# Performance work log

Measured on AMD Instinct MI355X. Metric: run time of the kernel, lower is better.

The kernel has to match this reference:

```python
import jax, jax.numpy as jnp
import numpy as np

D_MODEL = 512
HEAD_NUM = 8
EPS = 1e-5


def setup_inputs() -> dict:
    key = jax.random.key(0)
    ks = jax.random.split(key, 7)
    B, S, D = 2, 4096, D_MODEL
    scale = 1.0 / np.sqrt(D)
    return {
        "x": jax.random.normal(ks[0], (B, S, D), dtype=jnp.float32),
        "Wq": jax.random.normal(ks[1], (D, D), dtype=jnp.float32) * scale,
        "bq": jnp.zeros((D,), dtype=jnp.float32),
        "Wk": jax.random.normal(ks[2], (D, D), dtype=jnp.float32) * scale,
        "bk": jnp.zeros((D,), dtype=jnp.float32),
        "Wv": jax.random.normal(ks[3], (D, D), dtype=jnp.float32) * scale,
        "bv": jnp.zeros((D,), dtype=jnp.float32),
        "gamma": jnp.ones((D,), dtype=jnp.float32),
        "beta": jnp.zeros((D,), dtype=jnp.float32),
    }


def reference(x, Wq, bq, Wk, bk, Wv, bv, gamma, beta):
    B, S, D = x.shape
    H = HEAD_NUM
    hd = D // H  # q_k_head_dim == v_head_dim == 64
    q = (x @ Wq + bq).reshape(B, H, S, hd)  # faithful to torch .view (no transpose)
    k = (x @ Wk + bk).reshape(B, H, S, hd)
    v = (x @ Wv + bv).reshape(B, H, S, hd)
    # [B,H,S,S] score matrix, materialized exactly as the original does
    scores = jnp.einsum("bhqd,bhkd->bhqk", q, k) / jnp.sqrt(jnp.float32(hd))
    attn_w = jax.nn.softmax(scores, axis=-1)
    attn = jnp.einsum("bhqk,bhkd->bhqd", attn_w, v).reshape(B, S, D)
    h = x + attn
    mu = jnp.mean(h, axis=-1, keepdims=True)
    var = jnp.var(h, axis=-1, keepdims=True)
    y = (h - mu) / jnp.sqrt(var + EPS) * gamma + beta
    return y
```

## Files before the change

### kernel.cpp

```cpp
#include <hip/hip_runtime.h>
#include <stdint.h>

#define D_ 512
#define S_ 4096
#define HD 64
#define CHUNK (S_*HD)

typedef short short8 __attribute__((ext_vector_type(8)));
typedef unsigned short ushort8 __attribute__((ext_vector_type(8)));
typedef float f32x16 __attribute__((ext_vector_type(16)));
typedef float f32x4 __attribute__((ext_vector_type(4)));

__device__ __forceinline__ float b2f(unsigned short u){
  unsigned x = ((unsigned)u) << 16;
  return __builtin_bit_cast(float, x);
}
__device__ __forceinline__ unsigned short f2b(float f){
  unsigned x = __builtin_bit_cast(unsigned, f);
  return (unsigned short)((x + 0x7fffu + ((x >> 16) & 1u)) >> 16);
}
__device__ __forceinline__ unsigned cvt_pk_bf16(float lo, float hi){
  unsigned r; asm("v_cvt_pk_bf16_f32 %0, %1, %2" : "=v"(r) : "v"(lo), "v"(hi)); return r;
}
__device__ __forceinline__ float fexp2(float x){
  float r; asm("v_exp_f32 %0, %1" : "=v"(r) : "v"(x)); return r;
}

__global__ void k_convert_x(const float* __restrict__ x, unsigned short* __restrict__ xb){
  int i = blockIdx.x * blockDim.x + threadIdx.x;
  const float4* xv = (const float4*)x;
  float4 a = xv[i*2], b = xv[i*2+1];
  ushort8 o;
  o[0]=f2b(a.x); o[1]=f2b(a.y); o[2]=f2b(a.z); o[3]=f2b(a.w);
  o[4]=f2b(b.x); o[5]=f2b(b.y); o[6]=f2b(b.z); o[7]=f2b(b.w);
  ((ushort8*)xb)[i] = o;
}

__global__ void k_convert_w(const float* __restrict__ Wq, const float* __restrict__ Wk,
                            const float* __restrict__ Wv, unsigned short* __restrict__ wt){
  __shared__ __align__(16) float t[32][33];
  const float* W = (blockIdx.z==0) ? Wq : ((blockIdx.z==1) ? Wk : Wv);
  unsigned short* o = wt + blockIdx.z * D_ * D_;
  int k0 = blockIdx.x*32, n0 = blockIdx.y*32;
  int r = threadIdx.x >> 3, c4 = (threadIdx.x & 7) * 4;
  float4 vv = *(const float4*)&W[(k0+r)*D_ + n0 + c4];
  t[r][c4+0]=vv.x; t[r][c4+1]=vv.y; t[r][c4+2]=vv.z; t[r][c4+3]=vv.w;
  __syncthreads();
  unsigned short* dst = &o[(n0+r)*D_ + k0 + c4];
  dst[0]=f2b(t[c4+0][r]); dst[1]=f2b(t[c4+1][r]);
  dst[2]=f2b(t[c4+2][r]); dst[3]=f2b(t[c4+3][r]);
}

__global__ void __launch_bounds__(256) k_gemm(const unsigned short* __restrict__ xb,
                                              const unsigned short* __restrict__ wt,
                                              const float* __restrict__ bq,
                                              const float* __restrict__ bk,
                                              const float* __restrict__ bv,
                                              unsigned short* __restrict__ q,
                                              unsigned short* __restrict__ k,
                                              unsigned short* __restrict__ v){
  __shared__ __align__(16) unsigned short At[2][128*32];
  __shared__ __align__(16) unsigned short Bt[2][128*32];
  const int mat = blockIdx.z;
  const unsigned short* w = wt + mat * D_ * D_;
  const float* bias = (mat==0) ? bq : ((mat==1) ? bk : bv);
  unsigned short* out = (mat==0) ? q : ((mat==1) ? k : v);
  const int m0 = blockIdx.x * 128, n0 = blockIdx.y * 128;
  const int tid = threadIdx.x, lane = tid & 63, wv = tid >> 6;
  const int wm = wv >> 1, wn = wv & 1;
  const int l15 = lane & 15, l4 = lane >> 4;

  f32x4 acc[4][4] = {};

  auto stage = [&](int kt, int sel){
    const int kbase = kt * 32;
    #pragma unroll
    for (int j = 0; j < 2; j++){
      const int loff = wv*2048 + j*1024 + lane*16;
      const int row = loff >> 6;
      const int c = (loff >> 4) & 3;
      const int wb = row*64 + ((c ^ (row&3)) << 4);
      short8 av = *(const short8*)(xb + (m0+row)*D_ + kbase + (c<<3));
      short8 bv8 = *(const short8*)(w  + (n0+row)*D_ + kbase + (c<<3));
      *(short8*)((char*)At[sel] + wb) = av;
      *(short8*)((char*)Bt[sel] + wb) = bv8;
    }
  };

  stage(0, 0);
  int buf = 0;
  for (int kt = 0; kt < 16; ++kt){
    __syncthreads();
    if (kt + 1 < 16) stage(kt + 1, buf ^ 1);
    short8 af[4], bf[4];
    #pragma unroll
    for (int mf = 0; mf < 4; mf++){
      const int row = wm*64 + mf*16 + l15;
      af[mf] = *(const short8*)((const char*)At[buf] + row*64 + ((l4*16) ^ ((row&3)<<4)));
    }
    #pragma unroll
    for (int nf = 0; nf < 4; nf++){
      const int row = wn*64 + nf*16 + l15;
      bf[nf] = *(const short8*)((const char*)Bt[buf] + row*64 + ((l4*16) ^ ((row&3)<<4)));
    }
    #pragma unroll
    for (int mf = 0; mf < 4; mf++)
      #pragma unroll
      for (int nf = 0; nf < 4; nf++)
        acc[mf][nf] = __builtin_amdgcn_mfma_f32_16x16x32_bf16(af[mf], bf[nf], acc[mf][nf], 0,0,0);
    buf ^= 1;
  }
  #pragma unroll
  for (int nf = 0; nf < 4; nf++){
    const int n = n0 + wn*64 + nf*16 + l15;
    const float bval = bias[n];
    #pragma unroll
    for (int mf = 0; mf < 4; mf++){
      #pragma unroll
      for (int r = 0; r < 4; r++){
        const int m = m0 + wm*64 + mf*16 + l4*4 + r;
        out[m*D_ + n] = f2b(acc[mf][nf][r] + bval);
      }
    }
  }
}

__global__ void k_transpose_v(const unsigned short* __restrict__ v, unsigned short* __restrict__ vt){
  __shared__ __align__(16) unsigned short t[64][72];
  const int bh = blockIdx.y, s0 = blockIdx.x * 64;
  const unsigned short* vc = v + bh * CHUNK;
  unsigned short* vtc = vt + bh * CHUNK;
  const int tid = threadIdx.x;
  #pragma unroll
  for (int j = 0; j < 2; j++){
    const int e = j*2048 + tid*8;
    const int row = e >> 6, col = e & 63;
    *(ushort8*)&t[row][col] = *(const ushort8*)&vc[(s0+row)*HD + col];
  }
  __syncthreads();
  const int d = tid >> 2, sc0 = (tid & 3) * 16;
  ushort8 o0, o1;
  #pragma unroll
  for (int j = 0; j < 4; j++){
    o0[j]   = t[sc0 + j     ][d];
    o0[j+4] = t[sc0 + 8 + j ][d];
    o1[j]   = t[sc0 + 4 + j ][d];
    o1[j+4] = t[sc0 + 12 + j][d];
  }
  *(ushort8*)&vtc[d*S_ + s0 + sc0]     = o0;
  *(ushort8*)&vtc[d*S_ + s0 + sc0 + 8] = o1;
}

__global__ void __launch_bounds__(256) k_attn(const unsigned short* __restrict__ q,
                                              const unsigned short* __restrict__ k,
                                              const unsigned short* __restrict__ vt,
                                              const float* __restrict__ x,
                                              const float* __restrict__ gamma,
                                              const float* __restrict__ beta,
                                              float* __restrict__ out){
  __shared__ __align__(16) char smem[33280];
  const int tid = threadIdx.x, lane = tid & 63, wv = tid >> 6;
  const int l31 = lane & 31, hi = lane >> 5;
  const int bh = blockIdx.y;
  const unsigned short* qc  = q  + bh * CHUNK;
  const unsigned short* kc  = k  + bh * CHUNK;
  const unsigned short* vtc = vt + bh * CHUNK;
  const int q0 = blockIdx.x * 128 + wv * 32;

  short8 qf[4];
  {
    const int row = q0 + l31;
    #pragma unroll
    for (int kb = 0; kb < 4; kb++){
      ushort8 raw = *(const ushort8*)(qc + row*HD + kb*16 + hi*8);
      union { ushort8 u; short8 s; } c;
      #pragma unroll
      for (int j = 0; j < 8; j++) c.u[j] = f2b(b2f(raw[j]) * (0.125f * 1.44269504f));
      qf[kb] = c.s;
    }
  }

  f32x16 o0 = {}; f32x16 o1 = {};
  float mrun = -__builtin_inff(), lrun = 0.f;

  int srow[2], scol[2], swb[2];
  #pragma unroll
  for (int j = 0; j < 2; j++){
    const int loff = wv*2048 + j*1024 + lane*16;
    srow[j] = loff >> 7;
    scol[j] = (loff >> 4) & 7;
    swb[j]  = srow[j]*128 + ((scol[j] ^ (srow[j]&7)) << 4);
  }

  short8 kreg[2], vreg[2];
  auto stage_load = [&](int t){
    const int kv0 = t * 64;
    #pragma unroll
    for (int j = 0; j < 2; j++){
      kreg[j] = *(const short8*)(kc  + (kv0+srow[j])*HD + (scol[j]<<3));
      vreg[j] = *(const short8*)(vtc + srow[j]*S_ + kv0 + (scol[j]<<3));
    }
  };
  auto stage_write = [&](int sel){
    char* kb_ = smem + sel*8192;
    char* vb_ = smem + 16384 + sel*8192;
    #pragma unroll
    for (int j = 0; j < 2; j++){
      *(short8*)(kb_ + swb[j]) = kreg[j];
      *(short8*)(vb_ + swb[j]) = vreg[j];
    }
  };

  stage_load(0);
  stage_write(0);
  int buf = 0;
  const int NT = S_ / 64;
  for (int t = 0; t < NT; ++t){
    __syncthreads();
    if (t + 1 < NT) stage_load(t + 1);
    const char* kbuf = smem + buf*8192;
    const char* vbuf = smem + 16384 + buf*8192;

    f32x16 st0 = {}; f32x16 st1 = {};
    const int xr = (l31 & 7) << 4;
    #pragma unroll
    for (int kb = 0; kb < 4; kb++){
      const int off = kb*32 + hi*16;
      short8 kf0 = *(const short8*)(kbuf + l31*128        + (off ^ xr));
      short8 kf1 = *(const short8*)(kbuf + (32+l31)*128   + (off ^ xr));
      st0 = __builtin_amdgcn_mfma_f32_32x32x16_bf16(kf0, qf[kb], st0, 0,0,0);
      st1 = __builtin_amdgcn_mfma_f32_32x32x16_bf16(kf1, qf[kb], st1, 0,0,0);
    }

    float tm[8];
    #pragma unroll
    for (int r = 0; r < 8; r++) tm[r] = fmaxf(fmaxf(st0[r], st0[r+8]), fmaxf(st1[r], st1[r+8]));
    tm[0] = fmaxf(tm[0], tm[4]); tm[1] = fmaxf(tm[1], tm[5]);
    tm[2] = fmaxf(tm[2], tm[6]); tm[3] = fmaxf(tm[3], tm[7]);
    float pm = fmaxf(fmaxf(tm[0], tm[1]), fmaxf(tm[2], tm[3]));
    pm = fmaxf(pm, __shfl_xor(pm, 32));

    if (!__all(pm <= mrun + 10.0f)){
      const float mn = fmaxf(mrun, pm);
      const float corr = fexp2(mrun - mn);
      mrun = mn;
      lrun *= corr;
      o0 *= corr; o1 *= corr;
    }

    float s0a = 0.f, s1a = 0.f, s2a = 0.f, s3a = 0.f;
    #pragma unroll
    for (int r = 0; r < 8; r++){
      st0[r]   = fexp2(st0[r]   - mrun); s0a += st0[r];
      st0[r+8] = fexp2(st0[r+8] - mrun); s1a += st0[r+8];
      st1[r]   = fexp2(st1[r]   - mrun); s2a += st1[r];
      st1[r+8] = fexp2(st1[r+8] - mrun); s3a += st1[r+8];
    }
    float sum = (s0a + s1a) + (s2a + s3a);
    sum += __shfl_xor(sum, 32);
    lrun += sum;

    short8 pf[4];
    #pragma unroll
    for (int kb = 0; kb < 4; kb++){
      const f32x16& s = (kb < 2) ? st0 : st1;
      const int rb = (kb & 1) * 8;
      union { unsigned u[4]; short8 s8; } pu;
      pu.u[0] = cvt_pk_bf16(s[rb+0], s[rb+1]);
      pu.u[1] = cvt_pk_bf16(s[rb+2], s[rb+3]);
      pu.u[2] = cvt_pk_bf16(s[rb+4], s[rb+5]);
      pu.u[3] = cvt_pk_bf16(s[rb+6], s[rb+7]);
      pf[kb] = pu.s8;
    }

    #pragma unroll
    for (int kb = 0; kb < 4; kb++){
      const int off = kb*32 + hi*16;
      short8 vf0 = *(const short8*)(vbuf + l31*128      + (off ^ xr));
      short8 vf1 = *(const short8*)(vbuf + (32+l31)*128 + (off ^ xr));
      o0 = __builtin_amdgcn_mfma_f32_32x32x16_bf16(vf0, pf[kb], o0, 0,0,0);
      o1 = __builtin_amdgcn_mfma_f32_32x32x16_bf16(vf1, pf[kb], o1, 0,0,0);
    }

    if (t + 1 < NT) stage_write(buf ^ 1);
    buf ^= 1;
  }

  __syncthreads();
  {
    const float inv = 1.0f / lrun;
    float* po = (float*)(void*)smem + wv*2080;
    #pragma unroll
    for (int r = 0; r < 16; r++){
      const int d = (r&3) + 8*(r>>2) + 4*hi;
      po[l31*65 + d]      = o0[r] * inv;
      po[l31*65 + 32 + d] = o1[r] * inv;
    }
  }
  __syncthreads();
  {
    const float* po = (const float*)(void*)smem + wv*2080;
    const int s_sub = lane >> 3;
    const int dblk = (lane & 7) * 8;
    #pragma unroll
    for (int r = 0; r < 4; r++){
      const int R = bh*512 + (q0 >> 3) + r;
      const float* prow = po + (r*8 + s_sub)*65 + dblk;
      const float* xr2 = x + R*D_ + lane*8;
      float4 a0 = *(const float4*)xr2, a1 = *(const float4*)(xr2 + 4);
      float h[8];
      h[0]=a0.x+prow[0]; h[1]=a0.y+prow[1]; h[2]=a0.z+prow[2]; h[3]=a0.w+prow[3];
      h[4]=a1.x+prow[4]; h[5]=a1.y+prow[5]; h[6]=a1.z+prow[6]; h[7]=a1.w+prow[7];
      float s = 0.f, ss = 0.f;
      #pragma unroll
      for (int j = 0; j < 8; j++){ s += h[j]; ss += h[j]*h[j]; }
      #pragma unroll
      for (int msk = 1; msk < 64; msk <<= 1){ s += __shfl_xor(s, msk); ss += __shfl_xor(ss, msk); }
      const float mu = s * (1.f/512.f);
      const float var = ss * (1.f/512.f) - mu*mu;
      const float rs = rsqrtf(var + 1e-5f);
      const float* g = gamma + lane*8;
      const float* be = beta + lane*8;
      float4 w0, w1;
      w0.x = (h[0]-mu)*rs*g[0] + be[0];
      w0.y = (h[1]-mu)*rs*g[1] + be[1];
      w0.z = (h[2]-mu)*rs*g[2] + be[2];
      w0.w = (h[3]-mu)*rs*g[3] + be[3];
      w1.x = (h[4]-mu)*rs*g[4] + be[4];
      w1.y = (h[5]-mu)*rs*g[5] + be[5];
      w1.z = (h[6]-mu)*rs*g[6] + be[6];
      w1.w = (h[7]-mu)*rs*g[7] + be[7];
      float* op = out + R*D_ + lane*8;
      *(float4*)op = w0;
      *(float4*)(op + 4) = w1;
    }
  }
}

extern "C" void kernel_launch(void* const* d_in, const int* in_sizes, int n_in,
                              void* d_out, int out_size, void* d_ws, size_t ws_size,
                              hipStream_t stream){
  const float* x     = (const float*)d_in[0];
  const float* Wq    = (const float*)d_in[1];
  const float* bq    = (const float*)d_in[2];
  const float* Wk    = (const float*)d_in[3];
  const float* bk    = (const float*)d_in[4];
  const float* Wv    = (const float*)d_in[5];
  const float* bv    = (const float*)d_in[6];
  const float* gamma = (const float*)d_in[7];
  const float* beta  = (const float*)d_in[8];
  float* out = (float*)d_out;

  char* ws = (char*)d_ws;
  unsigned short* wt = (unsigned short*)(ws);
  unsigned short* q  = (unsigned short*)(ws + 1572864);
  unsigned short* k  = (unsigned short*)(ws + 9961472);
  unsigned short* v  = (unsigned short*)(ws + 18350080);
  unsigned short* vt = (unsigned short*)(ws + 26738688);
  unsigned short* xb = (unsigned short*)((char*)d_out + 8388608);

  k_convert_x  <<<2048, 256, 0, stream>>>(x, xb);
  k_convert_w  <<<dim3(16,16,3), 256, 0, stream>>>(Wq, Wk, Wv, wt);
  k_gemm       <<<dim3(64,4,3),  256, 0, stream>>>(xb, wt, bq, bk, bv, q, k, v);
  k_transpose_v<<<dim3(64,16),   256, 0, stream>>>(v, vt);
  k_attn       <<<dim3(32,16),   256, 0, stream>>>(q, k, vt, x, gamma, beta, out);
}
```

Before: 138.3 us.

## Split attention over KV halves and merge partials in a separate LayerNorm kernel

The attention kernel is split along the key/value dimension into two halves. This doubles the grid from 512 to 1024 blocks so more of the GPU's compute units are occupied, and the blocks are remapped with an XCD-aware index. Each half writes unnormalized bf16 partial outputs plus running max and sum. A new merge kernel combines the two halves with the log-sum-exp weights and applies the residual add and LayerNorm. MFMA sections are also wrapped in s_setprio. The cost is an extra launch, a global round-trip of the partials, and bf16 rounding of the partial outputs.

```diff
diff --git a/kernel.cpp b/kernel.cpp
--- a/kernel.cpp
+++ b/kernel.cpp
@@ -151,21 +151,29 @@
   *(ushort8*)&vtc[d*S_ + s0 + sc0 + 8] = o1;
 }
 
-__global__ void __launch_bounds__(256) k_attn(const unsigned short* __restrict__ q,
-                                              const unsigned short* __restrict__ k,
-                                              const unsigned short* __restrict__ vt,
-                                              const float* __restrict__ x,
-                                              const float* __restrict__ gamma,
-                                              const float* __restrict__ beta,
-                                              float* __restrict__ out){
+__global__ void __launch_bounds__(256) k_attn_part(const unsigned short* __restrict__ q,
+                                                   const unsigned short* __restrict__ k,
+                                                   const unsigned short* __restrict__ vt,
+                                                   unsigned short* __restrict__ Op0,
+                                                   unsigned short* __restrict__ Op1,
+                                                   float2* __restrict__ ml0,
+                                                   float2* __restrict__ ml1){
   __shared__ __align__(16) char smem[33280];
+  const int bid = blockIdx.x;
+  const int c8 = bid & 7, j = bid >> 3;
+  const int bh   = 2*c8 + (j & 1);
+  const int qblk = (j >> 1) & 31;
+  const int half = (j >> 6) & 1;
+
   const int tid = threadIdx.x, lane = tid & 63, wv = tid >> 6;
   const int l31 = lane & 31, hi = lane >> 5;
-  const int bh = blockIdx.y;
   const unsigned short* qc  = q  + bh * CHUNK;
   const unsigned short* kc  = k  + bh * CHUNK;
   const unsigned short* vtc = vt + bh * CHUNK;
-  const int q0 = blockIdx.x * 128 + wv * 32;
+  unsigned short* Op = half ? Op1 : Op0;
+  float2* ml = half ? ml1 : ml0;
+  const int q0 = qblk * 128 + wv * 32;
+  const int kvbase = half * 2048;
 
   short8 qf[4];
   {
@@ -173,10 +181,10 @@
     #pragma unroll
     for (int kb = 0; kb < 4; kb++){
       ushort8 raw = *(const ushort8*)(qc + row*HD + kb*16 + hi*8);
-      union { ushort8 u; short8 s; } c;
+      union { ushort8 u; short8 s; } cc;
       #pragma unroll
-      for (int j = 0; j < 8; j++) c.u[j] = f2b(b2f(raw[j]) * (0.125f * 1.44269504f));
-      qf[kb] = c.s;
+      for (int jj = 0; jj < 8; jj++) cc.u[jj] = f2b(b2f(raw[jj]) * (0.125f * 1.44269504f));
+      qf[kb] = cc.s;
     }
   }
 
@@ -185,36 +193,36 @@
 
   int srow[2], scol[2], swb[2];
   #pragma unroll
-  for (int j = 0; j < 2; j++){
-    const int loff = wv*2048 + j*1024 + lane*16;
-    srow[j] = loff >> 7;
-    scol[j] = (loff >> 4) & 7;
-    swb[j]  = srow[j]*128 + ((scol[j] ^ (srow[j]&7)) << 4);
+  for (int jj = 0; jj < 2; jj++){
+    const int loff = wv*2048 + jj*1024 + lane*16;
+    srow[jj] = loff >> 7;
+    scol[jj] = (loff >> 4) & 7;
+    swb[jj]  = srow[jj]*128 + ((scol[jj] ^ (srow[jj]&7)) << 4);
   }
 
   short8 kreg[2], vreg[2];
   auto stage_load = [&](int t){
-    const int kv0 = t * 64;
-    #pragma unroll
-    for (int j = 0; j < 2; j++){
-      kreg[j] = *(const short8*)(kc  + (kv0+srow[j])*HD + (scol[j]<<3));
-      vreg[j] = *(const short8*)(vtc + srow[j]*S_ + kv0 + (scol[j]<<3));
+    const int kv0 = kvbase + t * 64;
+    #pragma unroll
+    for (int jj = 0; jj < 2; jj++){
+      kreg[jj] = *(const short8*)(kc  + (kv0+srow[jj])*HD + (scol[jj]<<3));
+      vreg[jj] = *(const short8*)(vtc + srow[jj]*S_ + kv0 + (scol[jj]<<3));
     }
   };
   auto stage_write = [&](int sel){
     char* kb_ = smem + sel*8192;
     char* vb_ = smem + 16384 + sel*8192;
     #pragma unroll
-    for (int j = 0; j < 2; j++){
-      *(short8*)(kb_ + swb[j]) = kreg[j];
-      *(short8*)(vb_ + swb[j]) = vreg[j];
+    for (int jj = 0; jj < 2; jj++){
+      *(short8*)(kb_ + swb[jj]) = kreg[jj];
+      *(short8*)(vb_ + swb[jj]) = vreg[jj];
     }
   };
 
   stage_load(0);
   stage_write(0);
   int buf = 0;
-  const int NT = S_ / 64;
+  const int NT = 2048 / 64;
   for (int t = 0; t < NT; ++t){
     __syncthreads();
     if (t + 1 < NT) stage_load(t + 1);
@@ -223,6 +231,7 @@
 
     f32x16 st0 = {}; f32x16 st1 = {};
     const int xr = (l31 & 7) << 4;
+    __builtin_amdgcn_s_setprio(1);
     #pragma unroll
     for (int kb = 0; kb < 4; kb++){
       const int off = kb*32 + hi*16;
@@ -231,6 +240,7 @@
       st0 = __builtin_amdgcn_mfma_f32_32x32x16_bf16(kf0, qf[kb], st0, 0,0,0);
       st1 = __builtin_amdgcn_mfma_f32_32x32x16_bf16(kf1, qf[kb], st1, 0,0,0);
     }
+    __builtin_amdgcn_s_setprio(0);
 
     float tm[8];
     #pragma unroll
@@ -273,6 +283,7 @@
       pf[kb] = pu.s8;
     }
 
+    __builtin_amdgcn_s_setprio(1);
     #pragma unroll
     for (int kb = 0; kb < 4; kb++){
       const int off = kb*32 + hi*16;
@@ -281,6 +292,7 @@
       o0 = __builtin_amdgcn_mfma_f32_32x32x16_bf16(vf0, pf[kb], o0, 0,0,0);
       o1 = __builtin_amdgcn_mfma_f32_32x32x16_bf16(vf1, pf[kb], o1, 0,0,0);
     }
+    __builtin_amdgcn_s_setprio(0);
 
     if (t + 1 < NT) stage_write(buf ^ 1);
     buf ^= 1;
@@ -288,53 +300,84 @@
 
   __syncthreads();
   {
-    const float inv = 1.0f / lrun;
     float* po = (float*)(void*)smem + wv*2080;
     #pragma unroll
     for (int r = 0; r < 16; r++){
       const int d = (r&3) + 8*(r>>2) + 4*hi;
-      po[l31*65 + d]      = o0[r] * inv;
-      po[l31*65 + 32 + d] = o1[r] * inv;
-    }
+      po[l31*65 + d]      = o0[r];
+      po[l31*65 + 32 + d] = o1[r];
+    }
+  }
+  if (hi == 0){
+    ml[bh*S_ + q0 + l31] = make_float2(mrun, lrun);
   }
   __syncthreads();
   {
-    const float* po = (const float*)(void*)smem + wv*2080;
-    const int s_sub = lane >> 3;
-    const int dblk = (lane & 7) * 8;
-    #pragma unroll
-    for (int r = 0; r < 4; r++){
-      const int R = bh*512 + (q0 >> 3) + r;
-      const float* prow = po + (r*8 + s_sub)*65 + dblk;
-      const float* xr2 = x + R*D_ + lane*8;
-      float4 a0 = *(const float4*)xr2, a1 = *(const float4*)(xr2 + 4);
-      float h[8];
-      h[0]=a0.x+prow[0]; h[1]=a0.y+prow[1]; h[2]=a0.z+prow[2]; h[3]=a0.w+prow[3];
-      h[4]=a1.x+prow[4]; h[5]=a1.y+prow[5]; h[6]=a1.z+prow[6]; h[7]=a1.w+prow[7];
-      float s = 0.f, ss = 0.f;
+    const int rr = lane >> 1, hf = lane & 1;
+    const float* prow = (const float*)(void*)smem + wv*2080 + rr*65 + hf*32;
+    unsigned short* dst = Op + (bh*S_ + q0 + rr)*HD + hf*32;
+    #pragma unroll
+    for (int blk = 0; blk < 4; blk++){
+      ushort8 w8;
       #pragma unroll
-      for (int j = 0; j < 8; j++){ s += h[j]; ss += h[j]*h[j]; }
-      #pragma unroll
-      for (int msk = 1; msk < 64; msk <<= 1){ s += __shfl_xor(s, msk); ss += __shfl_xor(ss, msk); }
-      const float mu = s * (1.f/512.f);
-      const float var = ss * (1.f/512.f) - mu*mu;
-      const float rs = rsqrtf(var + 1e-5f);
-      const float* g = gamma + lane*8;
-      const float* be = beta + lane*8;
-      float4 w0, w1;
-      w0.x = (h[0]-mu)*rs*g[0] + be[0];
-      w0.y = (h[1]-mu)*rs*g[1] + be[1];
-      w0.z = (h[2]-mu)*rs*g[2] + be[2];
-      w0.w = (h[3]-mu)*rs*g[3] + be[3];
-      w1.x = (h[4]-mu)*rs*g[4] + be[4];
-      w1.y = (h[5]-mu)*rs*g[5] + be[5];
-      w1.z = (h[6]-mu)*rs*g[6] + be[6];
-      w1.w = (h[7]-mu)*rs*g[7] + be[7];
-      float* op = out + R*D_ + lane*8;
-      *(float4*)op = w0;
-      *(float4*)(op + 4) = w1;
-    }
-  }
+      for (int jj = 0; jj < 8; jj++) w8[jj] = f2b(prow[blk*8 + jj]);
+      *(ushort8*)(dst + blk*8) = w8;
+    }
+  }
+}
+
+__global__ void k_merge_ln(const unsigned short* __restrict__ Op0,
+                           const unsigned short* __restrict__ Op1,
+                           const float2* __restrict__ ml0,
+                           const float2* __restrict__ ml1,
+                           const float* __restrict__ x,
+                           const float* __restrict__ gamma,
+                           const float* __restrict__ beta,
+                           float* __restrict__ out){
+  const int row = blockIdx.x * 4 + (threadIdx.x >> 6);
+  const int lane = threadIdx.x & 63;
+  const int bh = row >> 9;
+  const int s_attn = ((row & 511) << 3) + (lane >> 3);
+  const int d0 = (lane & 7) * 8;
+  const int oidx = (bh*S_ + s_attn)*HD + d0;
+  ushort8 u0 = *(const ushort8*)(Op0 + oidx);
+  ushort8 u1 = *(const ushort8*)(Op1 + oidx);
+  const float2 a = ml0[bh*S_ + s_attn];
+  const float2 c = ml1[bh*S_ + s_attn];
+  const float M  = fmaxf(a.x, c.x);
+  const float e1 = exp2f(a.x - M), e2 = exp2f(c.x - M);
+  const float inv = 1.0f / (e1*a.y + e2*c.y);
+  const float w1 = e1 * inv, w2 = e2 * inv;
+
+  const float* xr = x + row*D_ + lane*8;
+  float4 a0 = *(const float4*)xr, a1 = *(const float4*)(xr + 4);
+  float h[8];
+  h[0]=a0.x; h[1]=a0.y; h[2]=a0.z; h[3]=a0.w; h[4]=a1.x; h[5]=a1.y; h[6]=a1.z; h[7]=a1.w;
+  #pragma unroll
+  for (int jj = 0; jj < 8; jj++) h[jj] += w1*b2f(u0[jj]) + w2*b2f(u1[jj]);
+
+  float sm = 0.f, ss = 0.f;
+  #pragma unroll
+  for (int jj = 0; jj < 8; jj++){ sm += h[jj]; ss += h[jj]*h[jj]; }
+  #pragma unroll
+  for (int msk = 1; msk < 64; msk <<= 1){ sm += __shfl_xor(sm, msk); ss += __shfl_xor(ss, msk); }
+  const float mu = sm * (1.f/512.f);
+  const float var = ss * (1.f/512.f) - mu*mu;
+  const float rs = rsqrtf(var + 1e-5f);
+  const float* g = gamma + lane*8;
+  const float* be = beta + lane*8;
+  float4 w0, w3;
+  w0.x = (h[0]-mu)*rs*g[0] + be[0];
+  w0.y = (h[1]-mu)*rs*g[1] + be[1];
+  w0.z = (h[2]-mu)*rs*g[2] + be[2];
+  w0.w = (h[3]-mu)*rs*g[3] + be[3];
+  w3.x = (h[4]-mu)*rs*g[4] + be[4];
+  w3.y = (h[5]-mu)*rs*g[5] + be[5];
+  w3.z = (h[6]-mu)*rs*g[6] + be[6];
+  w3.w = (h[7]-mu)*rs*g[7] + be[7];
+  float* op = out + row*D_ + lane*8;
+  *(float4*)op = w0;
+  *(float4*)(op + 4) = w3;
 }
 
 extern "C" void kernel_launch(void* const* d_in, const int* in_sizes, int n_in,
@@ -357,11 +400,16 @@
   unsigned short* k  = (unsigned short*)(ws + 9961472);
   unsigned short* v  = (unsigned short*)(ws + 18350080);
   unsigned short* vt = (unsigned short*)(ws + 26738688);
+  unsigned short* Op0 = v;
+  unsigned short* Op1 = (unsigned short*)(ws + 35127296);
+  float2* ml0 = (float2*)(ws + 43515904);
+  float2* ml1 = (float2*)(ws + 44040192);
   unsigned short* xb = (unsigned short*)((char*)d_out + 8388608);
 
   k_convert_x  <<<2048, 256, 0, stream>>>(x, xb);
   k_convert_w  <<<dim3(16,16,3), 256, 0, stream>>>(Wq, Wk, Wv, wt);
   k_gemm       <<<dim3(64,4,3),  256, 0, stream>>>(xb, wt, bq, bk, bv, q, k, v);
   k_transpose_v<<<dim3(64,16),   256, 0, stream>>>(v, vt);
-  k_attn       <<<dim3(32,16),   256, 0, stream>>>(q, k, vt, x, gamma, beta, out);
-}
+  k_attn_part  <<<1024, 256, 0, stream>>>(q, k, vt, Op0, Op1, ml0, ml1);
+  k_merge_ln   <<<2048, 256, 0, stream>>>(Op0, Op1, ml0, ml1, x, gamma, beta, out);
+}
```

Measured after the change: 146.7 us. 6.1% more time.
